# Kernel optimization log

Measured on AMD Instinct MI355X. Metric: run time of the kernel, lower is better.

The kernel has to match this reference:

```python
import jax, jax.numpy as jnp
import numpy as np

H, Hh, E, V, OUT, B, S, T, PAD = 512, 256, 512, 50000, 512, 64, 128, 128, 0


def setup_inputs() -> dict:
    key = jax.random.key(0)
    ks = iter(jax.random.split(key, 32))

    def p(shape, scale=0.05):
        return jax.random.normal(next(ks), shape, jnp.float32) * scale

    emb_in = p((V, E)).at[PAD].set(0.0)   # padding_idx row is zero
    emb_out = p((V, E)).at[PAD].set(0.0)
    src_tokens = jax.random.randint(next(ks), (B, S), 1, V)  # avoid pad_idx=0
    dst = jax.random.randint(next(ks), (B, T), 1, V)
    return {
        'src_tokens': src_tokens,
        'src_lengths': jnp.full((B,), S, dtype=jnp.int32),  # full lengths -> pack/pad is identity
        'dst': dst,
        'emb_in': emb_in, 'emb_out': emb_out,
        'enc_w_ih0': p((2, 4 * Hh, E)),   # [dir, 4h, in] layer0
        'enc_w_ih1': p((2, 4 * Hh, H)),   # layer1 input is bidir concat (H)
        'enc_w_hh': p((2, 2, 4 * Hh, Hh)),  # [layer, dir, 4h, h]
        'enc_b_ih': p((2, 2, 4 * Hh)),
        'enc_b_hh': p((2, 2, 4 * Hh)),
        'dec_w_ih0': p((4 * H, H + E)), 'dec_w_hh0': p((4 * H, H)),
        'dec_b_ih0': p((4 * H,)), 'dec_b_hh0': p((4 * H,)),
        'dec_w_ih1': p((4 * H, H)), 'dec_w_hh1': p((4 * H, H)),
        'dec_b_ih1': p((4 * H,)), 'dec_b_hh1': p((4 * H,)),
        'attn_w': p((H, 2 * H)),           # output_proj, bias=False
        'pred_w': p((OUT, H)), 'pred_b': p((OUT,)),
    }


def _lstm_cell(x, h, c, w_ih, w_hh, b_ih, b_hh):
    # torch gate order: i, f, g, o
    g = x @ w_ih.T + h @ w_hh.T + b_ih + b_hh
    i, f, gg, o = jnp.split(g, 4, axis=-1)
    c = jax.nn.sigmoid(f) * c + jax.nn.sigmoid(i) * jnp.tanh(gg)
    h = jax.nn.sigmoid(o) * jnp.tanh(c)
    return h, c


def _run_lstm(xs, w_ih, w_hh, b_ih, b_hh, reverse):
    z = jnp.zeros((xs.shape[1], w_hh.shape[1]), xs.dtype)

    def step(carry, x):
        h, c = _lstm_cell(x, carry[0], carry[1], w_ih, w_hh, b_ih, b_hh)
        return (h, c), h

    (h, c), out = jax.lax.scan(step, (z, z), xs, reverse=reverse)
    return out, h, c


def _forward(src_tokens, dst, emb_in, emb_out, enc_w_ih0, enc_w_ih1, enc_w_hh,
             enc_b_ih, enc_b_hh, dec_w_ih0, dec_w_hh0, dec_b_ih0, dec_b_hh0,
             dec_w_ih1, dec_w_hh1, dec_b_ih1, dec_b_hh1, attn_w, pred_w, pred_b):
    src = src_tokens.T          # [S, B]
    dst_t = dst.T               # [T, B]
    bsz = src.shape[1]

    # ---- Encoder: 2-layer bidirectional LSTM (sequences are full length) ----
    x = emb_in[src]             # [S, B, E]
    w_ihs = (enc_w_ih0, enc_w_ih1)
    fin_h, fin_c = [], []
    for l in range(2):
        outs = []
        for d, rev in ((0, False), (1, True)):
            o, h, c = _run_lstm(x, w_ihs[l][d], enc_w_hh[l, d], enc_b_ih[l, d], enc_b_hh[l, d], rev)
            outs.append(o)
            fin_h.append(h)
            fin_c.append(c)
        x = jnp.concatenate(outs, axis=-1)   # [S, B, H]
    enc_out = x
    # combine_bidir: per-layer concat of fwd/bwd final states -> [B, H]
    h_l0 = jnp.concatenate(fin_h[0:2], axis=-1)
    h_l1 = jnp.concatenate(fin_h[2:4], axis=-1)
    c_l0 = jnp.concatenate(fin_c[0:2], axis=-1)
    c_l1 = jnp.concatenate(fin_c[2:4], axis=-1)

    enc_mask = (src == PAD)     # [S, B]
    dst_emb = emb_out[dst_t]    # [T, B, E]

    # ---- Decoder: 2 stacked LSTMCells + dot-product attention, input feeding ----
    def dec_step(carry, emb_t):
        h0, c0, h1, c1, feed = carry
        inp = jnp.concatenate((emb_t, feed), axis=1)          # [B, E+H]
        h0, c0 = _lstm_cell(inp, h0, c0, dec_w_ih0, dec_w_hh0, dec_b_ih0, dec_b_hh0)
        h1, c1 = _lstm_cell(h0, h1, c1, dec_w_ih1, dec_w_hh1, dec_b_ih1, dec_b_hh1)
        scores = jnp.einsum('sbh,bh->sb', enc_out, h1)        # [S, B]
        scores = jnp.where(enc_mask, -jnp.inf, scores)
        attn = jax.nn.softmax(scores, axis=0)
        ctx = jnp.einsum('sb,sbh->bh', attn, enc_out)         # [B, H]
        out = jnp.tanh(jnp.concatenate((ctx, h1), axis=1) @ attn_w.T)
        return (h0, c0, h1, c1, out), out

    feed0 = jnp.zeros((bsz, H), dst_emb.dtype)
    _, outs = jax.lax.scan(dec_step, (h_l0, c_l0, h_l1, c_l1, feed0), dst_emb)  # [T, B, H]

    # pred_proj then transpose(1, 2) -> [B, OUT, T]
    res = jnp.einsum('tbh,oh->bot', outs, pred_w) + pred_b[None, :, None]
    return res


def reference(src_tokens, src_lengths, dst, emb_in, emb_out, enc_w_ih0, enc_w_ih1,
              enc_w_hh, enc_b_ih, enc_b_hh, dec_w_ih0, dec_w_hh0, dec_b_ih0,
              dec_b_hh0, dec_w_ih1, dec_w_hh1, dec_b_ih1, dec_b_hh1, attn_w,
              pred_w, pred_b):
    # src_lengths are all == S so pack_padded/pad_packed is an identity
    del src_lengths
    return _forward(src_tokens, dst, emb_in, emb_out, enc_w_ih0, enc_w_ih1,
                    enc_w_hh, enc_b_ih, enc_b_hh, dec_w_ih0, dec_w_hh0,
                    dec_b_ih0, dec_b_hh0, dec_w_ih1, dec_w_hh1, dec_b_ih1,
                    dec_b_hh1, attn_w, pred_w, pred_b)
```

## Files before the change

kernel.cpp:

```cpp
#include <hip/hip_runtime.h>
#include <hip/hip_bf16.h>

#define SS 128
#define TT 128
#define NBLK 256
#define NBD  128
#define FSTRIDE 16

typedef __attribute__((ext_vector_type(8))) short bf16x8;
typedef __attribute__((ext_vector_type(4))) float f32x4;
typedef unsigned short ushort_t;

__device__ __forceinline__ float sigf(float x) { return 1.f / (1.f + __expf(-x)); }

__device__ __forceinline__ ushort_t f2bf(float f) {
  unsigned b = __builtin_bit_cast(unsigned, f);
  return (ushort_t)((b + 0x7FFFu + ((b >> 16) & 1u)) >> 16);
}
__device__ __forceinline__ float bf2f(ushort_t u) {
  return __builtin_bit_cast(float, (unsigned)u << 16);
}

__device__ __forceinline__ void cstoreh(ushort_t* p, ushort_t v) {
  __hip_atomic_store(p, v, __ATOMIC_RELAXED, __HIP_MEMORY_SCOPE_AGENT);
}

__device__ __forceinline__ int xidx(int k, int b) {
  return (((k >> 5) * 256 + b * 4 + ((k >> 3) & 3)) << 3) + (k & 7);
}

template<int NB>
__device__ __forceinline__ void gbar(unsigned* flags, unsigned gen) {
  __syncthreads();
  int tid = threadIdx.x;
  unsigned* arr = flags;
  unsigned* go  = flags + NB * FSTRIDE;
  if (blockIdx.x == 0) {
    if (tid > 0 && tid < NB) {
      int guard = 0;
      while (__hip_atomic_load(&arr[tid * FSTRIDE], __ATOMIC_RELAXED,
                               __HIP_MEMORY_SCOPE_AGENT) < gen &&
             ++guard < (1 << 20))
        __builtin_amdgcn_s_sleep(1);
    }
    __syncthreads();
    if (tid < NB)
      __hip_atomic_store(&go[tid * FSTRIDE], gen, __ATOMIC_RELAXED,
                         __HIP_MEMORY_SCOPE_AGENT);
  } else {
    if (tid == 0) {
      asm volatile("s_waitcnt vmcnt(0)" ::: "memory");
      __hip_atomic_store(&arr[blockIdx.x * FSTRIDE], gen, __ATOMIC_RELAXED,
                         __HIP_MEMORY_SCOPE_AGENT);
      int guard = 0;
      while (__hip_atomic_load(&go[blockIdx.x * FSTRIDE], __ATOMIC_RELAXED,
                               __HIP_MEMORY_SCOPE_AGENT) < gen &&
             ++guard < (1 << 20))
        __builtin_amdgcn_s_sleep(1);
    }
    __syncthreads();
  }
  asm volatile("" ::: "memory");
}

__global__ void k_embed_bf(const float* __restrict__ emb, const int* __restrict__ toks,
                           ushort_t* __restrict__ out, int seqlen) {
  int s = blockIdx.x >> 6, b = blockIdx.x & 63;
  int tok = toks[b * seqlen + s];
  float4 v = ((const float4*)(emb + (size_t)tok * 512))[threadIdx.x];
  unsigned lo = (unsigned)f2bf(v.x) | ((unsigned)f2bf(v.y) << 16);
  unsigned hi = (unsigned)f2bf(v.z) | ((unsigned)f2bf(v.w) << 16);
  uint2 pk = {lo, hi};
  *(uint2*)&out[(size_t)blockIdx.x * 512 + threadIdx.x * 4] = pk;
}

__global__ void k_castw(const float* __restrict__ s0, const float* __restrict__ s1,
                        const float* __restrict__ s2, const float* __restrict__ s3,
                        ushort_t* __restrict__ wBF, ushort_t* __restrict__ predBF) {
  int row = blockIdx.x, which = blockIdx.y;
  if (which == 3 && row >= 512) return;
  const float* src = (which == 0) ? s0 + (size_t)row * 512
                   : (which == 1) ? s1 + (size_t)row * 512
                   : (which == 2) ? s2 + (size_t)row * 1024
                                  : s3 + (size_t)row * 512;
  float4 v = ((const float4*)src)[threadIdx.x];
  unsigned lo = (unsigned)f2bf(v.x) | ((unsigned)f2bf(v.y) << 16);
  unsigned hi = (unsigned)f2bf(v.z) | ((unsigned)f2bf(v.w) << 16);
  uint2 pk = {lo, hi};
  if (which == 3)
    *(uint2*)&predBF[(size_t)row * 512 + threadIdx.x * 4] = pk;
  else
    *(uint2*)&wBF[((size_t)which * 2048 + row) * 512 + threadIdx.x * 4] = pk;
}

__global__ __launch_bounds__(256) void gemm_bf(
    const ushort_t* __restrict__ X, const ushort_t* __restrict__ W,
    const float* __restrict__ b1, const float* __restrict__ b2,
    float* __restrict__ C, int MODE) {
  __shared__ ushort_t Xs[128 * 72];
  __shared__ ushort_t Ws[128 * 72];
  __shared__ float sbias[128];
  int n0 = blockIdx.x * 128, m0 = blockIdx.y * 128;
  int tid = threadIdx.x;
  int lane = tid & 63;
  int wv = __builtin_amdgcn_readfirstlane(tid >> 6);
  int h_m = (wv >> 1) * 64, h_n = (wv & 1) * 64;
  int l16 = lane & 15, l4 = (lane >> 4) * 4, k8 = (lane >> 4) * 8;
  if (tid < 128) sbias[tid] = b1[n0 + tid] + (b2 ? b2[n0 + tid] : 0.f);
  f32x4 acc[4][4] = {};
  int lrow = tid >> 1, lhf = (tid & 1) * 32;
  for (int k0 = 0; k0 < 512; k0 += 64) {
    __syncthreads();
    const ushort_t* xs = X + (size_t)(m0 + lrow) * 512 + k0 + lhf;
    const ushort_t* wsrc = W + (size_t)(n0 + lrow) * 512 + k0 + lhf;
#pragma unroll
    for (int q = 0; q < 4; ++q) {
      *(bf16x8*)&Xs[lrow * 72 + lhf + q * 8] = *(const bf16x8*)(xs + q * 8);
      *(bf16x8*)&Ws[lrow * 72 + lhf + q * 8] = *(const bf16x8*)(wsrc + q * 8);
    }
    __syncthreads();
#pragma unroll
    for (int kk = 0; kk < 2; ++kk) {
#pragma unroll
      for (int mt = 0; mt < 4; ++mt) {
        bf16x8 af = *(const bf16x8*)&Xs[(h_m + mt * 16 + l16) * 72 + kk * 32 + k8];
#pragma unroll
        for (int nt = 0; nt < 4; ++nt) {
          bf16x8 bf = *(const bf16x8*)&Ws[(h_n + nt * 16 + l16) * 72 + kk * 32 + k8];
          acc[mt][nt] = __builtin_amdgcn_mfma_f32_16x16x32_bf16(af, bf, acc[mt][nt], 0, 0, 0);
        }
      }
    }
  }
  if (MODE == 1) {
    int s = (m0 + h_m) >> 6;
#pragma unroll
    for (int nt = 0; nt < 4; ++nt) {
      int n = n0 + h_n + nt * 16 + l16;
      float bias = sbias[h_n + nt * 16 + l16];
#pragma unroll
      for (int mt = 0; mt < 4; ++mt) {
        f32x4 v = acc[mt][nt];
        v[0] += bias; v[1] += bias; v[2] += bias; v[3] += bias;
        *(f32x4*)&C[((size_t)s * 2048 + n) * 64 + mt * 16 + l4] = v;
      }
    }
  } else {
#pragma unroll
    for (int nt = 0; nt < 4; ++nt) {
      int n = n0 + h_n + nt * 16 + l16;
      float bias = sbias[h_n + nt * 16 + l16];
#pragma unroll
      for (int mt = 0; mt < 4; ++mt) {
#pragma unroll
        for (int r = 0; r < 4; ++r) {
          int m = m0 + h_m + mt * 16 + l4 + r;
          C[((size_t)(m & 63) * 512 + n) * 128 + (m >> 6)] = acc[mt][nt][r] + bias;
        }
      }
    }
  }
}

template<int LOUT>
__global__ __launch_bounds__(256, 1) void enc_persist(
    const float* __restrict__ GT,
    const float* __restrict__ whh,
    ushort_t* __restrict__ ringE,
    ushort_t* __restrict__ lout,
    ushort_t* __restrict__ hFin,
    float* __restrict__ cFin,
    unsigned* bar) {
  int nb = blockIdx.x;
  int d = nb >> 7, nbL = nb & 127;
  int tid = threadIdx.x;
  int lane = tid & 63;
  int wv = __builtin_amdgcn_readfirstlane(tid >> 6);
  int l16 = lane & 15, kg = lane >> 4;
  __shared__ ushort_t wE[16 * 264];

  for (int idx = tid; idx < 16 * 256; idx += 256) {
    int m = idx >> 8, k = idx & 255;
    float v = 0.f;
    if (m < 8)
      v = whh[(size_t)d * 262144 +
              (size_t)((m & 3) * 256 + nbL + 128 * (m >> 2)) * 256 + k];
    wE[m * 264 + k] = f2bf(v);
  }
  __syncthreads();

  int b = wv * 16 + l16;
  int hu = nbL + 128 * kg;
  float creg = 0.f;
  const ushort_t* wp = wE + l16 * 264 + kg * 8;

  for (int t = 0; t < SS; ++t) {
    int s = d ? (SS - 1 - t) : t;
    const ushort_t* xb = ringE + (size_t)(t * 2 + d) * 16384 +
                         wv * 512 + l16 * 32 + kg * 8;
    bf16x8 bfr[8];
#pragma unroll
    for (int ks = 0; ks < 8; ++ks) bfr[ks] = *(const bf16x8*)(xb + ks * 2048);
    float gi[4];
    if (lane < 32) {
#pragma unroll
      for (int r = 0; r < 4; ++r)
        gi[r] = GT[((size_t)s * 2048 + d * 1024 + r * 256 + hu) * 64 + b];
    }
    f32x4 acc = {0.f, 0.f, 0.f, 0.f};
#pragma unroll
    for (int ks = 0; ks < 8; ++ks) {
      bf16x8 af = *(const bf16x8*)(wp + ks * 32);
      acc = __builtin_amdgcn_mfma_f32_16x16x32_bf16(af, bfr[ks], acc, 0, 0, 0);
    }
    if (lane < 32) {
      float g4[4];
#pragma unroll
      for (int r = 0; r < 4; ++r) g4[r] = acc[r] + gi[r];
      float ig = sigf(g4[0]), fg = sigf(g4[1]), gg = tanhf(g4[2]), og = sigf(g4[3]);
      creg = fg * creg + ig * gg;
      float hn = og * tanhf(creg);
      cstoreh(&ringE[(size_t)((t + 1) * 2 + d) * 16384 + xidx(hu, b)], f2bf(hn));
      if (LOUT == 0)
        lout[((size_t)s * 64 + b) * 512 + d * 256 + hu] = f2bf(hn);
      else
        lout[(size_t)b * 65536 + (size_t)s * 512 + d * 256 + hu] = f2bf(hn);
      if (t == SS - 1) {
        hFin[xidx(512 + d * 256 + hu, b)] = f2bf(hn);
        cFin[(d * 256 + hu) * 64 + b] = creg;
      }
    }
    if (t < SS - 1) gbar<NBLK>(bar, (unsigned)(t + 1));
  }
}

__global__ __launch_bounds__(256, 1) void dec_persist(
    const float* __restrict__ GdT,
    const float* __restrict__ w_ih0, const float* __restrict__ w_hh0,
    const float* __restrict__ w_ih1, const float* __restrict__ w_hh1,
    const float* __restrict__ b_ih1, const float* __restrict__ b_hh1,
    const float* __restrict__ attn_w,
    const ushort_t* __restrict__ enc_out,
    const int* __restrict__ src_tokens,
    const float* __restrict__ c0T, const float* __restrict__ c1T,
    ushort_t* __restrict__ r0, ushort_t* __restrict__ r1,
    ushort_t* __restrict__ r2,
    ushort_t* __restrict__ houtsB,
    unsigned* bar) {
  int nb = blockIdx.x;
  int tid = threadIdx.x;
  int lane = tid & 63;
  int wv = __builtin_amdgcn_readfirstlane(tid >> 6);
  int l16 = lane & 15, kg = lane >> 4;
  __shared__ ushort_t wAl[16 * 1032];
  __shared__ ushort_t wBl[16 * 1032];
  __shared__ ushort_t wDl[16 * 1032];
  __shared__ float h1s[512];
  __shared__ float sc[128];

  for (int idx = tid; idx < 16384; idx += 256) {
    int m = idx >> 10, k = idx & 1023;
    int j = m >> 2, g = m & 3;
    int row = g * 512 + nb + 128 * j;
    float va = (k < 512) ? w_ih0[(size_t)row * 1024 + 512 + k]
                         : w_hh0[(size_t)row * 512 + (k - 512)];
    float vb = (k < 512) ? w_ih1[(size_t)row * 512 + k]
                         : w_hh1[(size_t)row * 512 + (k - 512)];
    float vd = (m < 4) ? attn_w[(size_t)(nb * 4 + m) * 1024 + k] : 0.f;
    wAl[m * 1032 + k] = f2bf(va);
    wBl[m * 1032 + k] = f2bf(vb);
    wDl[m * 1032 + k] = f2bf(vd);
  }
  __syncthreads();

  int b = wv * 16 + l16;
  int hu = nb + 128 * kg;
  float c0r = c0T[hu * 64 + b];
  float c1r = c1T[hu * 64 + b];
  float bias1[4];
#pragma unroll
  for (int r = 0; r < 4; ++r)
    bias1[r] = b_ih1[r * 512 + hu] + b_hh1[r * 512 + hu];
  const ushort_t* wpA = wAl + l16 * 1032 + kg * 8;
  const ushort_t* wpB = wBl + l16 * 1032 + kg * 8;
  const ushort_t* wpD = wDl + l16 * 1032 + kg * 8;
  int fragoff = wv * 512 + l16 * 32 + kg * 8;

  for (int t = 0; t < TT; ++t) {
    unsigned gb = (unsigned)(t * 4);
    size_t sC = (size_t)t * 65536, sN = (size_t)(t + 1) * 65536;
    {
      const ushort_t* xb = r0 + sC + fragoff;
      bf16x8 bfr[32];
#pragma unroll
      for (int ks = 0; ks < 32; ++ks) bfr[ks] = *(const bf16x8*)(xb + ks * 2048);
      float giA[4];
#pragma unroll
      for (int r = 0; r < 4; ++r)
        giA[r] = GdT[((size_t)t * 2048 + r * 512 + hu) * 64 + b];
      f32x4 acc = {0.f, 0.f, 0.f, 0.f};
#pragma unroll
      for (int ks = 0; ks < 32; ++ks) {
        bf16x8 af = *(const bf16x8*)(wpA + ks * 32);
        acc = __builtin_amdgcn_mfma_f32_16x16x32_bf16(af, bfr[ks], acc, 0, 0, 0);
      }
      float g4[4];
#pragma unroll
      for (int r = 0; r < 4; ++r) g4[r] = acc[r] + giA[r];
      float ig = sigf(g4[0]), fg = sigf(g4[1]), gg = tanhf(g4[2]), og = sigf(g4[3]);
      c0r = fg * c0r + ig * gg;
      float hn = og * tanhf(c0r);
      cstoreh(&r0[sN + xidx(512 + hu, b)], f2bf(hn));
    }
    gbar<NBD>(bar, gb + 1);
    {
      bf16x8 bfr[32];
      const ushort_t* xh0 = r0 + sN + fragoff;
      const ushort_t* xh1 = r1 + sC + fragoff;
#pragma unroll
      for (int ks = 0; ks < 16; ++ks) bfr[ks] = *(const bf16x8*)(xh0 + (16 + ks) * 2048);
#pragma unroll
      for (int ks = 16; ks < 32; ++ks) bfr[ks] = *(const bf16x8*)(xh1 + ks * 2048);
      f32x4 acc = {0.f, 0.f, 0.f, 0.f};
#pragma unroll
      for (int ks = 0; ks < 32; ++ks) {
        bf16x8 af = *(const bf16x8*)(wpB + ks * 32);
        acc = __builtin_amdgcn_mfma_f32_16x16x32_bf16(af, bfr[ks], acc, 0, 0, 0);
      }
      float g4[4];
#pragma unroll
      for (int r = 0; r < 4; ++r) g4[r] = acc[r] + bias1[r];
      float ig = sigf(g4[0]), fg = sigf(g4[1]), gg = tanhf(g4[2]), og = sigf(g4[3]);
      c1r = fg * c1r + ig * gg;
      float hn = og * tanhf(c1r);
      cstoreh(&r1[sN + xidx(512 + hu, b)], f2bf(hn));
    }
    gbar<NBD>(bar, gb + 2);
    if (nb < 64) {
      const ushort_t* eb = enc_out + (size_t)nb * 65536;
      for (int i = tid; i < 512; i += 256)
        h1s[i] = bf2f(r1[sN + xidx(512 + i, nb)]);
      __syncthreads();
      {
        int s2 = tid >> 1, half = tid & 1;
        const ushort_t* er = eb + (size_t)s2 * 512 + half * 256;
        const float* hh = h1s + half * 256;
        float a = 0.f;
#pragma unroll 4
        for (int k = 0; k < 256; k += 8) {
          bf16x8 ev = *(const bf16x8*)(er + k);
#pragma unroll
          for (int i = 0; i < 8; ++i)
            a += bf2f((ushort_t)ev[i]) * hh[k + i];
        }
        a += __shfl_xor(a, 1);
        if (!half) sc[s2] = (src_tokens[nb * SS + s2] == 0) ? -1e30f : a;
      }
      __syncthreads();
      if (tid < 64) {
        float m = fmaxf(sc[tid], sc[tid + 64]);
        for (int off = 32; off; off >>= 1) m = fmaxf(m, __shfl_xor(m, off));
        float e0 = __expf(sc[tid] - m), e1 = __expf(sc[tid + 64] - m);
        float ssum = e0 + e1;
        for (int off = 32; off; off >>= 1) ssum += __shfl_xor(ssum, off);
        float inv = 1.f / ssum;
        sc[tid] = e0 * inv; sc[tid + 64] = e1 * inv;
      }
      __syncthreads();
      float a0 = 0.f, a1 = 0.f;
      for (int s2 = 0; s2 < 128; ++s2) {
        float p_ = sc[s2];
        const ushort_t* er = eb + (size_t)s2 * 512;
        a0 += p_ * bf2f(er[tid]);
        a1 += p_ * bf2f(er[tid + 256]);
      }
      cstoreh(&r2[sC + xidx(tid, nb)], f2bf(a0));
      cstoreh(&r2[sC + xidx(tid + 256, nb)], f2bf(a1));
    }
    gbar<NBD>(bar, gb + 3);
    {
      bf16x8 bfr[32];
      const ushort_t* xc = r2 + sC + fragoff;
      const ushort_t* xh1 = r1 + sN + fragoff;
#pragma unroll
      for (int ks = 0; ks < 16; ++ks) bfr[ks] = *(const bf16x8*)(xc + ks * 2048);
#pragma unroll
      for (int ks = 16; ks < 32; ++ks) bfr[ks] = *(const bf16x8*)(xh1 + ks * 2048);
      f32x4 acc = {0.f, 0.f, 0.f, 0.f};
#pragma unroll
      for (int ks = 0; ks < 32; ++ks) {
        bf16x8 af = *(const bf16x8*)(wpD + ks * 32);
        acc = __builtin_amdgcn_mfma_f32_16x16x32_bf16(af, bfr[ks], acc, 0, 0, 0);
      }
      if (lane < 16) {
#pragma unroll
        for (int r = 0; r < 4; ++r) {
          int o = nb * 4 + r;
          float v = tanhf(acc[r]);
          ushort_t vb = f2bf(v);
          cstoreh(&r0[sN + xidx(o, b)], vb);
          houtsB[((size_t)t * 64 + b) * 512 + o] = vb;
        }
      }
    }
    if (t < TT - 1) gbar<NBD>(bar, gb + 4);
  }
}

extern "C" void kernel_launch(void* const* d_in, const int* in_sizes, int n_in,
                              void* d_out, int out_size, void* d_ws, size_t ws_size,
                              hipStream_t stream) {
  const int*   src_tokens = (const int*)d_in[0];
  const int*   dst        = (const int*)d_in[2];
  const float* emb_in     = (const float*)d_in[3];
  const float* emb_out    = (const float*)d_in[4];
  const float* enc_w_ih0  = (const float*)d_in[5];
  const float* enc_w_ih1  = (const float*)d_in[6];
  const float* enc_w_hh   = (const float*)d_in[7];
  const float* enc_b_ih   = (const float*)d_in[8];
  const float* enc_b_hh   = (const float*)d_in[9];
  const float* dec_w_ih0  = (const float*)d_in[10];
  const float* dec_w_hh0  = (const float*)d_in[11];
  const float* dec_b_ih0  = (const float*)d_in[12];
  const float* dec_b_hh0  = (const float*)d_in[13];
  const float* dec_w_ih1  = (const float*)d_in[14];
  const float* dec_w_hh1  = (const float*)d_in[15];
  const float* dec_b_ih1  = (const float*)d_in[16];
  const float* dec_b_hh1  = (const float*)d_in[17];
  const float* attn_w     = (const float*)d_in[18];
  const float* pred_w     = (const float*)d_in[19];
  const float* pred_b     = (const float*)d_in[20];
  float* out = (float*)d_out;

  float* ws       = (float*)d_ws;
  ushort_t* houtsB = (ushort_t*)ws;
  float* GT       = ws + 4194304;
  ushort_t* encOutB = (ushort_t*)(ws + 20971520);
  ushort_t* predBF  = (ushort_t*)(ws + 23068672);
  ushort_t* r0    = (ushort_t*)(ws + 25165824);
  ushort_t* r1    = (ushort_t*)(ws + 29392896);
  ushort_t* r2    = (ushort_t*)(ws + 33619968);
  ushort_t* wBF   = r2;
  ushort_t* ringE = (ushort_t*)(ws + 37814272);
  float* c0T      = ws + 39927808;
  float* c1T      = ws + 39960576;
  unsigned* barA  = (unsigned*)(ws + 39993344);
  unsigned* barB  = barA + 8192;
  unsigned* barC  = barB + 8192;
  ushort_t* U     = (ushort_t*)(ws + 40017920);

  hipMemsetAsync(barA, 0, 3 * 8192 * sizeof(unsigned), stream);
  hipMemsetAsync(r0, 0, 65536 * sizeof(ushort_t), stream);
  hipMemsetAsync(r1, 0, 65536 * sizeof(ushort_t), stream);
  hipMemsetAsync(ringE, 0, 32768 * sizeof(ushort_t), stream);

  k_castw<<<dim3(2048, 4), 128, 0, stream>>>(enc_w_ih0, enc_w_ih1, dec_w_ih0,
                                             pred_w, wBF, predBF);

  k_embed_bf<<<dim3(8192), 128, 0, stream>>>(emb_in, src_tokens, U, SS);
  gemm_bf<<<dim3(16, 64), 256, 0, stream>>>(U, wBF, enc_b_ih, enc_b_hh, GT, 1);
  enc_persist<0><<<dim3(NBLK), 256, 0, stream>>>(GT, enc_w_hh, ringE, U,
                                                 r0, c0T, barA);
  gemm_bf<<<dim3(16, 64), 256, 0, stream>>>(U, wBF + 1048576,
                                            enc_b_ih + 2048, enc_b_hh + 2048, GT, 1);
  enc_persist<1><<<dim3(NBLK), 256, 0, stream>>>(GT, enc_w_hh + 524288, ringE,
                                                 encOutB, r1, c1T, barB);

  k_embed_bf<<<dim3(8192), 128, 0, stream>>>(emb_out, dst, U, TT);
  gemm_bf<<<dim3(16, 64), 256, 0, stream>>>(U, wBF + 2097152,
                                            dec_b_ih0, dec_b_hh0, GT, 1);

  dec_persist<<<dim3(NBD), 256, 0, stream>>>(
      GT, dec_w_ih0, dec_w_hh0, dec_w_ih1, dec_w_hh1, dec_b_ih1, dec_b_hh1,
      attn_w, encOutB, src_tokens, c0T, c1T, r0, r1, r2, houtsB, barC);

  gemm_bf<<<dim3(4, 64), 256, 0, stream>>>(houtsB, predBF,
                                           pred_b, nullptr, out, 2);
}
```

Before: 4.320 ms.

## Halve decoder persistent blocks, giving each block two hidden-unit tiles

The persistent decoder kernel now runs on 64 blocks instead of 128. Each block holds twice as many LSTM gate weight rows in LDS and issues two MFMA chains per step, and the attention output projection covers 8 rows per block with half the A fragment zero-padded. Fewer participants in each grid-wide barrier should make the several barriers per timestep cheaper, and all blocks now do attention work. In exchange each block does twice the matrix work per step on fewer CUs and uses more LDS.

Measured after the change: 4.345 ms. Within noise of the previous version (+0.6%).

```diff
diff --git a/kernel.cpp b/kernel.cpp
--- a/kernel.cpp
+++ b/kernel.cpp
@@ -4,7 +4,7 @@
 #define SS 128
 #define TT 128
 #define NBLK 256
-#define NBD  128
+#define NBD  64
 #define FSTRIDE 16
 
 typedef __attribute__((ext_vector_type(8))) short bf16x8;
@@ -252,38 +252,45 @@
   int lane = tid & 63;
   int wv = __builtin_amdgcn_readfirstlane(tid >> 6);
   int l16 = lane & 15, kg = lane >> 4;
-  __shared__ ushort_t wAl[16 * 1032];
-  __shared__ ushort_t wBl[16 * 1032];
-  __shared__ ushort_t wDl[16 * 1032];
+  __shared__ ushort_t wAl[32 * 1032];
+  __shared__ ushort_t wBl[32 * 1032];
+  __shared__ ushort_t wDl[8 * 1032];
   __shared__ float h1s[512];
   __shared__ float sc[128];
 
-  for (int idx = tid; idx < 16384; idx += 256) {
+  for (int idx = tid; idx < 32768; idx += 256) {
     int m = idx >> 10, k = idx & 1023;
     int j = m >> 2, g = m & 3;
-    int row = g * 512 + nb + 128 * j;
+    int row = g * 512 + nb + 64 * j;
     float va = (k < 512) ? w_ih0[(size_t)row * 1024 + 512 + k]
                          : w_hh0[(size_t)row * 512 + (k - 512)];
     float vb = (k < 512) ? w_ih1[(size_t)row * 512 + k]
                          : w_hh1[(size_t)row * 512 + (k - 512)];
-    float vd = (m < 4) ? attn_w[(size_t)(nb * 4 + m) * 1024 + k] : 0.f;
     wAl[m * 1032 + k] = f2bf(va);
     wBl[m * 1032 + k] = f2bf(vb);
-    wDl[m * 1032 + k] = f2bf(vd);
+  }
+  for (int idx = tid; idx < 8192; idx += 256) {
+    int m = idx >> 10, k = idx & 1023;
+    wDl[m * 1032 + k] = f2bf(attn_w[(size_t)(nb * 8 + m) * 1024 + k]);
   }
   __syncthreads();
 
   int b = wv * 16 + l16;
-  int hu = nb + 128 * kg;
-  float c0r = c0T[hu * 64 + b];
-  float c1r = c1T[hu * 64 + b];
-  float bias1[4];
-#pragma unroll
-  for (int r = 0; r < 4; ++r)
-    bias1[r] = b_ih1[r * 512 + hu] + b_hh1[r * 512 + hu];
-  const ushort_t* wpA = wAl + l16 * 1032 + kg * 8;
-  const ushort_t* wpB = wBl + l16 * 1032 + kg * 8;
-  const ushort_t* wpD = wDl + l16 * 1032 + kg * 8;
+  int hu0 = nb + 64 * kg;
+  int hu1 = nb + 64 * (kg + 4);
+  float c0r[2], c1r[2], bias1[2][4];
+  c0r[0] = c0T[hu0 * 64 + b]; c0r[1] = c0T[hu1 * 64 + b];
+  c1r[0] = c1T[hu0 * 64 + b]; c1r[1] = c1T[hu1 * 64 + b];
+#pragma unroll
+  for (int r = 0; r < 4; ++r) {
+    bias1[0][r] = b_ih1[r * 512 + hu0] + b_hh1[r * 512 + hu0];
+    bias1[1][r] = b_ih1[r * 512 + hu1] + b_hh1[r * 512 + hu1];
+  }
+  const ushort_t* wpA0 = wAl + l16 * 1032 + kg * 8;
+  const ushort_t* wpA1 = wAl + (16 + l16) * 1032 + kg * 8;
+  const ushort_t* wpB0 = wBl + l16 * 1032 + kg * 8;
+  const ushort_t* wpB1 = wBl + (16 + l16) * 1032 + kg * 8;
+  const ushort_t* wpD  = wDl + l16 * 1032 + kg * 8;
   int fragoff = wv * 512 + l16 * 32 + kg * 8;
 
   for (int t = 0; t < TT; ++t) {
@@ -294,23 +301,30 @@
       bf16x8 bfr[32];
 #pragma unroll
       for (int ks = 0; ks < 32; ++ks) bfr[ks] = *(const bf16x8*)(xb + ks * 2048);
-      float giA[4];
-#pragma unroll
-      for (int r = 0; r < 4; ++r)
-        giA[r] = GdT[((size_t)t * 2048 + r * 512 + hu) * 64 + b];
-      f32x4 acc = {0.f, 0.f, 0.f, 0.f};
+      float giA[2][4];
+#pragma unroll
+      for (int r = 0; r < 4; ++r) {
+        giA[0][r] = GdT[((size_t)t * 2048 + r * 512 + hu0) * 64 + b];
+        giA[1][r] = GdT[((size_t)t * 2048 + r * 512 + hu1) * 64 + b];
+      }
+      f32x4 a0 = {0.f, 0.f, 0.f, 0.f}, a1 = {0.f, 0.f, 0.f, 0.f};
 #pragma unroll
       for (int ks = 0; ks < 32; ++ks) {
-        bf16x8 af = *(const bf16x8*)(wpA + ks * 32);
-        acc = __builtin_amdgcn_mfma_f32_16x16x32_bf16(af, bfr[ks], acc, 0, 0, 0);
-      }
-      float g4[4];
-#pragma unroll
-      for (int r = 0; r < 4; ++r) g4[r] = acc[r] + giA[r];
-      float ig = sigf(g4[0]), fg = sigf(g4[1]), gg = tanhf(g4[2]), og = sigf(g4[3]);
-      c0r = fg * c0r + ig * gg;
-      float hn = og * tanhf(c0r);
-      cstoreh(&r0[sN + xidx(512 + hu, b)], f2bf(hn));
+        a0 = __builtin_amdgcn_mfma_f32_16x16x32_bf16(
+            *(const bf16x8*)(wpA0 + ks * 32), bfr[ks], a0, 0, 0, 0);
+        a1 = __builtin_amdgcn_mfma_f32_16x16x32_bf16(
+            *(const bf16x8*)(wpA1 + ks * 32), bfr[ks], a1, 0, 0, 0);
+      }
+#pragma unroll
+      for (int T = 0; T < 2; ++T) {
+        f32x4 acc = T ? a1 : a0;
+        int hu = T ? hu1 : hu0;
+        float ig = sigf(acc[0] + giA[T][0]), fg = sigf(acc[1] + giA[T][1]);
+        float gg = tanhf(acc[2] + giA[T][2]), og = sigf(acc[3] + giA[T][3]);
+        c0r[T] = fg * c0r[T] + ig * gg;
+        float hn = og * tanhf(c0r[T]);
+        cstoreh(&r0[sN + xidx(512 + hu, b)], f2bf(hn));
+      }
     }
     gbar<NBD>(bar, gb + 1);
     {
@@ -321,22 +335,27 @@
       for (int ks = 0; ks < 16; ++ks) bfr[ks] = *(const bf16x8*)(xh0 + (16 + ks) * 2048);
 #pragma unroll
       for (int ks = 16; ks < 32; ++ks) bfr[ks] = *(const bf16x8*)(xh1 + ks * 2048);
-      f32x4 acc = {0.f, 0.f, 0.f, 0.f};
+      f32x4 a0 = {0.f, 0.f, 0.f, 0.f}, a1 = {0.f, 0.f, 0.f, 0.f};
 #pragma unroll
       for (int ks = 0; ks < 32; ++ks) {
-        bf16x8 af = *(const bf16x8*)(wpB + ks * 32);
-        acc = __builtin_amdgcn_mfma_f32_16x16x32_bf16(af, bfr[ks], acc, 0, 0, 0);
-      }
-      float g4[4];
-#pragma unroll
-      for (int r = 0; r < 4; ++r) g4[r] = acc[r] + bias1[r];
-      float ig = sigf(g4[0]), fg = sigf(g4[1]), gg = tanhf(g4[2]), og = sigf(g4[3]);
-      c1r = fg * c1r + ig * gg;
-      float hn = og * tanhf(c1r);
-      cstoreh(&r1[sN + xidx(512 + hu, b)], f2bf(hn));
+        a0 = __builtin_amdgcn_mfma_f32_16x16x32_bf16(
+            *(const bf16x8*)(wpB0 + ks * 32), bfr[ks], a0, 0, 0, 0);
+        a1 = __builtin_amdgcn_mfma_f32_16x16x32_bf16(
+            *(const bf16x8*)(wpB1 + ks * 32), bfr[ks], a1, 0, 0, 0);
+      }
+#pragma unroll
+      for (int T = 0; T < 2; ++T) {
+        f32x4 acc = T ? a1 : a0;
+        int hu = T ? hu1 : hu0;
+        float ig = sigf(acc[0] + bias1[T][0]), fg = sigf(acc[1] + bias1[T][1]);
+        float gg = tanhf(acc[2] + bias1[T][2]), og = sigf(acc[3] + bias1[T][3]);
+        c1r[T] = fg * c1r[T] + ig * gg;
+        float hn = og * tanhf(c1r[T]);
+        cstoreh(&r1[sN + xidx(512 + hu, b)], f2bf(hn));
+      }
     }
     gbar<NBD>(bar, gb + 2);
-    if (nb < 64) {
+    {
       const ushort_t* eb = enc_out + (size_t)nb * 65536;
       for (int i = tid; i < 512; i += 256)
         h1s[i] = bf2f(r1[sN + xidx(512 + i, nb)]);
@@ -387,15 +406,16 @@
 #pragma unroll
       for (int ks = 16; ks < 32; ++ks) bfr[ks] = *(const bf16x8*)(xh1 + ks * 2048);
       f32x4 acc = {0.f, 0.f, 0.f, 0.f};
+      bf16x8 zf = {};
 #pragma unroll
       for (int ks = 0; ks < 32; ++ks) {
-        bf16x8 af = *(const bf16x8*)(wpD + ks * 32);
+        bf16x8 af = (l16 < 8) ? *(const bf16x8*)(wpD + ks * 32) : zf;
         acc = __builtin_amdgcn_mfma_f32_16x16x32_bf16(af, bfr[ks], acc, 0, 0, 0);
       }
-      if (lane < 16) {
+      if (kg < 2) {
 #pragma unroll
         for (int r = 0; r < 4; ++r) {
-          int o = nb * 4 + r;
+          int o = nb * 8 + kg * 4 + r;
           float v = tanhf(acc[r]);
           ushort_t vb = f2bf(v);
           cstoreh(&r0[sN + xidx(o, b)], vb);
```
